# Performance work log

Hardware: AMD Instinct MI355X
Metric: run time of the kernel (lower is better)

Reference implementation:

```python
import jax, jax.numpy as jnp
import numpy as np

T, H, E, I, SI, TOP_K = 4096, 2048, 16, 1024, 4096, 1


def setup_inputs() -> dict:
    key = jax.random.key(0)
    ks = jax.random.split(key, 8)
    s_h = 1.0 / np.sqrt(H)
    s_i = 1.0 / np.sqrt(I)
    s_si = 1.0 / np.sqrt(SI)
    return {
        "hidden_states": jax.random.normal(ks[0], (T, H), jnp.float32),
        "router_w": jax.random.normal(ks[1], (E, H), jnp.float32) * s_h,
        "w_gate": jax.random.normal(ks[2], (E, H, I), jnp.float32) * s_h,
        "w_up": jax.random.normal(ks[3], (E, H, I), jnp.float32) * s_h,
        "w_down": jax.random.normal(ks[4], (E, I, H), jnp.float32) * s_i,
        "ws_gate": jax.random.normal(ks[5], (H, SI), jnp.float32) * s_h,
        "ws_up": jax.random.normal(ks[6], (H, SI), jnp.float32) * s_h,
        "ws_down": jax.random.normal(ks[7], (SI, H), jnp.float32) * s_si,
    }


def reference(hidden_states, router_w, w_gate, w_up, w_down, ws_gate, ws_up, ws_down):
    x = hidden_states  # [T, H]
    # Router: logits -> top-k -> sigmoid weights (Llama4RenormalizeMoeRoutingMethod)
    logits = jnp.einsum("th,eh->te", x, router_w)              # [T, E]
    top_vals, top_idx = jax.lax.top_k(logits, TOP_K)            # [T, K]
    weights = jax.nn.sigmoid(top_vals)                          # [T, K]
    # dispatch[t, e] = router weight if expert e selected for token t, else 0
    onehot = jax.nn.one_hot(top_idx, E, dtype=x.dtype)          # [T, K, E]
    dispatch = jnp.einsum("tke,tk->te", onehot, weights)        # [T, E]
    # Routed experts: router weight applied on input (commutes through the
    # linear gate/up projections as a per-(t,e) scalar applied before SiLU).
    g = jnp.einsum("th,ehi->tei", x, w_gate) * dispatch[:, :, None]  # [T, E, I]
    u = jnp.einsum("th,ehi->tei", x, w_up) * dispatch[:, :, None]    # [T, E, I]
    act = jax.nn.silu(g) * u                                          # [T, E, I]
    # Unselected experts contribute exactly 0 (act==0 there), so summing over
    # E in the down projection is the combine step.
    routed = jnp.einsum("tei,eih->th", act, w_down)             # [T, H]
    # Shared expert (SiLU-gated MLP on the unscaled hidden states)
    shared = (jax.nn.silu(x @ ws_gate) * (x @ ws_up)) @ ws_down  # [T, H]
    return shared + routed
```

## Files before the change

### kernel.cpp

```cpp
#include <hip/hip_runtime.h>
#include <hip/hip_bf16.h>

typedef unsigned short u16;
typedef unsigned int   u32;
typedef __attribute__((ext_vector_type(8))) short short8;
typedef __attribute__((ext_vector_type(4))) float f32x4;

#define T_TOK 4096
#define HDIM  2048
#define NEXP  16
#define IDIM  1024
#define SIDIM 4096
#define RCAP  6144
#define NTIL  48

#define O_WT      0u
#define O_EIDX    16384u
#define O_CNT     32768u
#define O_POS     32832u
#define O_PADOFF  32896u
#define O_TILEEXP 33024u
#define O_TOKROW  33280u
#define O_XBF     65536u
#define O_XSC     (O_XBF + 2u*T_TOK*HDIM)
#define O_ACTS    (O_XSC + 2u*RCAP*HDIM)
#define O_ACTR    (O_ACTS + 2u*T_TOK*SIDIM)

__device__ __forceinline__ u16 f2b(float f) {
  u32 u = __float_as_uint(f);
  u = (u + 0x7FFFu + ((u >> 16) & 1u)) >> 16;
  return (u16)u;
}

__global__ __launch_bounds__(256) void router_k(
    const float* __restrict__ x, const float* __restrict__ rw,
    float* __restrict__ wt, int* __restrict__ eidx, int* __restrict__ cnt) {
  int w = threadIdx.x >> 6, l = threadIdx.x & 63;
  int t = blockIdx.x * 4 + w;
  double acc[NEXP];
#pragma unroll
  for (int e = 0; e < NEXP; ++e) acc[e] = 0.0;
  const float* xp = x + (size_t)t * HDIM;
  for (int hb = 0; hb < HDIM; hb += 256) {
    float4 xv = *(const float4*)(xp + hb + l * 4);
#pragma unroll
    for (int e = 0; e < NEXP; ++e) {
      float4 wv = *(const float4*)(rw + (size_t)e * HDIM + hb + l * 4);
      acc[e] += (double)xv.x * wv.x + (double)xv.y * wv.y
              + (double)xv.z * wv.z + (double)xv.w * wv.w;
    }
  }
#pragma unroll
  for (int e = 0; e < NEXP; ++e) {
    double v = acc[e];
#pragma unroll
    for (int off = 32; off; off >>= 1) v += __shfl_xor(v, off, 64);
    acc[e] = v;
  }
  if (l == 0) {
    double best = acc[0]; int be = 0;
#pragma unroll
    for (int e = 1; e < NEXP; ++e) if (acc[e] > best) { best = acc[e]; be = e; }
    wt[t] = 1.0f / (1.0f + __expf(-(float)best));
    eidx[t] = be;
    atomicAdd(&cnt[be], 1);
  }
}

__global__ void scan_k(const int* __restrict__ cnt, int* __restrict__ pad_off,
                       int* __restrict__ tile_exp, int* __restrict__ pos,
                       int* __restrict__ tok_row) {
  if (threadIdx.x == 0) {
    for (int i = 0; i < 64; ++i) tile_exp[i] = -1;
    int run = 0;
    for (int e = 0; e < NEXP; ++e) {
      pad_off[e] = run;
      int pc = ((cnt[e] + 127) >> 7) << 7;
      for (int tt = run >> 7; tt < (run + pc) >> 7; ++tt) tile_exp[tt] = e;
      run += pc;
      pos[e] = 0;
    }
    pad_off[NEXP] = run;
  }
  for (int i = threadIdx.x; i < RCAP; i += 256) tok_row[i] = -1;
}

__global__ void assign_k(const int* __restrict__ eidx, const int* __restrict__ pad_off,
                         int* __restrict__ pos, int* __restrict__ tok_row) {
  int t = blockIdx.x * 256 + threadIdx.x;
  if (t >= T_TOK) return;
  int e = eidx[t];
  int r = atomicAdd(&pos[e], 1);
  tok_row[pad_off[e] + r] = t;
}

__global__ __launch_bounds__(256) void cvt_k(
    const float* __restrict__ x, const float* __restrict__ wt,
    const int* __restrict__ tok_row, u16* __restrict__ xbf, u16* __restrict__ xsc) {
  int row = blockIdx.x;
  int tid = threadIdx.x;
  if (row < T_TOK) {
    const float* src = x + (size_t)row * HDIM;
    u16* dst = xbf + (size_t)row * HDIM;
#pragma unroll
    for (int i = 0; i < 2; ++i) {
      int c = i * 1024 + tid * 4;
      float4 v = *(const float4*)(src + c);
      uint2 o;
      o.x = (u32)f2b(v.x) | ((u32)f2b(v.y) << 16);
      o.y = (u32)f2b(v.z) | ((u32)f2b(v.w) << 16);
      *(uint2*)(dst + c) = o;
    }
  } else {
    int g = row - T_TOK;
    u16* dst = xsc + (size_t)g * HDIM;
    int t = tok_row[g];
    if (t < 0) {
      uint2 z; z.x = 0u; z.y = 0u;
#pragma unroll
      for (int i = 0; i < 2; ++i) *(uint2*)(dst + i * 1024 + tid * 4) = z;
    } else {
      float s = wt[t];
      const float* src = x + (size_t)t * HDIM;
#pragma unroll
      for (int i = 0; i < 2; ++i) {
        int c = i * 1024 + tid * 4;
        float4 v = *(const float4*)(src + c);
        uint2 o;
        o.x = (u32)f2b(v.x * s) | ((u32)f2b(v.y * s) << 16);
        o.y = (u32)f2b(v.z * s) | ((u32)f2b(v.w * s) << 16);
        *(uint2*)(dst + c) = o;
      }
    }
  }
}


template<bool ROUTED>
__global__ __launch_bounds__(256) void gemm_gu(
    const u16* __restrict__ A, int lda,
    const float* __restrict__ Bg0, const float* __restrict__ Bu0, int ldb,
    int K, u16* __restrict__ act, int ldact,
    const int* __restrict__ tile_exp) {
  __shared__ __align__(16) u16 As[128 * 64];
  __shared__ __align__(16) u16 Bgs[64 * 72];
  __shared__ __align__(16) u16 Bus[64 * 72];
  const int tid = threadIdx.x;
  const int w = tid >> 6, l = tid & 63;
  const int wm = w >> 1, wn = w & 1;
  const int m0 = blockIdx.y * 128, n0 = blockIdx.x * 64;
  const float* Bg = Bg0;
  const float* Bu = Bu0;
  if (ROUTED) {
    int e = tile_exp[blockIdx.y];
    if (e < 0) return;
    size_t off = (size_t)e * (size_t)K * (size_t)ldb;
    Bg += off; Bu += off;
  }
  f32x4 accg[4][2], accu[4][2];
#pragma unroll
  for (int i = 0; i < 4; ++i)
#pragma unroll
    for (int j = 0; j < 2; ++j)
#pragma unroll
      for (int r = 0; r < 4; ++r) { accg[i][j][r] = 0.0f; accu[i][j][r] = 0.0f; }

  const int ra = tid >> 3;
  const int ca = (tid & 7) * 8;
  const u16* Ab = A + (size_t)m0 * lda;

  for (int k0 = 0; k0 < K; k0 += 64) {
    __syncthreads();
#pragma unroll
    for (int i = 0; i < 4; ++i) {
      int r = ra + 32 * i;
      int4 v = *(const int4*)(Ab + (size_t)r * lda + k0 + ca);
      *(int4*)&As[r * 64 + (ca ^ ((r & 7) * 8))] = v;
    }
    {
      const float* bp = Bg + (size_t)(k0 + w * 16) * ldb + n0 + l;
      u16 h[16];
#pragma unroll
      for (int i = 0; i < 16; ++i) h[i] = f2b(bp[(size_t)i * ldb]);
#pragma unroll
      for (int j = 0; j < 4; ++j) {
        uint2 v; v.x = (u32)h[4*j] | ((u32)h[4*j+1] << 16);
        v.y = (u32)h[4*j+2] | ((u32)h[4*j+3] << 16);
        *(uint2*)&Bgs[l * 72 + w * 16 + j * 4] = v;
      }
      bp = Bu + (size_t)(k0 + w * 16) * ldb + n0 + l;
#pragma unroll
      for (int i = 0; i < 16; ++i) h[i] = f2b(bp[(size_t)i * ldb]);
#pragma unroll
      for (int j = 0; j < 4; ++j) {
        uint2 v; v.x = (u32)h[4*j] | ((u32)h[4*j+1] << 16);
        v.y = (u32)h[4*j+2] | ((u32)h[4*j+3] << 16);
        *(uint2*)&Bus[l * 72 + w * 16 + j * 4] = v;
      }
    }
    __syncthreads();
#pragma unroll
    for (int kh = 0; kh < 2; ++kh) {
      short8 af[4];
#pragma unroll
      for (int mf = 0; mf < 4; ++mf) {
        int r = wm * 64 + mf * 16 + (l & 15);
        int c = (kh * 32 + (l >> 4) * 8) ^ ((r & 7) * 8);
        af[mf] = *(const short8*)&As[r * 64 + c];
      }
      short8 bgf[2], buf2[2];
#pragma unroll
      for (int nf = 0; nf < 2; ++nf) {
        int n = wn * 32 + nf * 16 + (l & 15);
        int c = kh * 32 + (l >> 4) * 8;
        bgf[nf]  = *(const short8*)&Bgs[n * 72 + c];
        buf2[nf] = *(const short8*)&Bus[n * 72 + c];
      }
#pragma unroll
      for (int mf = 0; mf < 4; ++mf)
#pragma unroll
        for (int nf = 0; nf < 2; ++nf) {
          accg[mf][nf] = __builtin_amdgcn_mfma_f32_16x16x32_bf16(af[mf], bgf[nf],  accg[mf][nf], 0, 0, 0);
          accu[mf][nf] = __builtin_amdgcn_mfma_f32_16x16x32_bf16(af[mf], buf2[nf], accu[mf][nf], 0, 0, 0);
        }
    }
  }
#pragma unroll
  for (int mf = 0; mf < 4; ++mf)
#pragma unroll
    for (int nf = 0; nf < 2; ++nf) {
      int col = n0 + wn * 32 + nf * 16 + (l & 15);
#pragma unroll
      for (int r = 0; r < 4; ++r) {
        int row = m0 + wm * 64 + mf * 16 + (l >> 4) * 4 + r;
        float g = accg[mf][nf][r], u = accu[mf][nf][r];
        float s = g / (1.0f + __expf(-g));
        act[(size_t)row * ldact + col] = f2b(s * u);
      }
    }
}

template<bool ROUTED>
__global__ __launch_bounds__(256) void gemm_down(
    const u16* __restrict__ A, int lda,
    const float* __restrict__ B0, int ldb, int K,
    float* __restrict__ out, int ldout,
    const int* __restrict__ tile_exp, const int* __restrict__ tok_row) {
  __shared__ __align__(16) u16 As[128 * 64];
  __shared__ __align__(16) u16 Bs[64 * 72];
  const int tid = threadIdx.x;
  const int w = tid >> 6, l = tid & 63;
  const int wm = w >> 1, wn = w & 1;
  const int m0 = blockIdx.y * 128, n0 = blockIdx.x * 64;
  const float* B = B0;
  if (ROUTED) {
    int e = tile_exp[blockIdx.y];
    if (e < 0) return;
    B += (size_t)e * (size_t)K * (size_t)ldb;
  }
  f32x4 acc[4][2];
#pragma unroll
  for (int i = 0; i < 4; ++i)
#pragma unroll
    for (int j = 0; j < 2; ++j)
#pragma unroll
      for (int r = 0; r < 4; ++r) acc[i][j][r] = 0.0f;

  const int ra = tid >> 3;
  const int ca = (tid & 7) * 8;
  const u16* Ab = A + (size_t)m0 * lda;

  for (int k0 = 0; k0 < K; k0 += 64) {
    __syncthreads();
#pragma unroll
    for (int i = 0; i < 4; ++i) {
      int r = ra + 32 * i;
      int4 v = *(const int4*)(Ab + (size_t)r * lda + k0 + ca);
      *(int4*)&As[r * 64 + (ca ^ ((r & 7) * 8))] = v;
    }
    {
      const float* bp = B + (size_t)(k0 + w * 16) * ldb + n0 + l;
      u16 h[16];
#pragma unroll
      for (int i = 0; i < 16; ++i) h[i] = f2b(bp[(size_t)i * ldb]);
#pragma unroll
      for (int j = 0; j < 4; ++j) {
        uint2 v; v.x = (u32)h[4*j] | ((u32)h[4*j+1] << 16);
        v.y = (u32)h[4*j+2] | ((u32)h[4*j+3] << 16);
        *(uint2*)&Bs[l * 72 + w * 16 + j * 4] = v;
      }
    }
    __syncthreads();
#pragma unroll
    for (int kh = 0; kh < 2; ++kh) {
      short8 af[4];
#pragma unroll
      for (int mf = 0; mf < 4; ++mf) {
        int r = wm * 64 + mf * 16 + (l & 15);
        int c = (kh * 32 + (l >> 4) * 8) ^ ((r & 7) * 8);
        af[mf] = *(const short8*)&As[r * 64 + c];
      }
      short8 bf[2];
#pragma unroll
      for (int nf = 0; nf < 2; ++nf) {
        int n = wn * 32 + nf * 16 + (l & 15);
        int c = kh * 32 + (l >> 4) * 8;
        bf[nf] = *(const short8*)&Bs[n * 72 + c];
      }
#pragma unroll
      for (int mf = 0; mf < 4; ++mf)
#pragma unroll
        for (int nf = 0; nf < 2; ++nf)
          acc[mf][nf] = __builtin_amdgcn_mfma_f32_16x16x32_bf16(af[mf], bf[nf], acc[mf][nf], 0, 0, 0);
    }
  }
#pragma unroll
  for (int mf = 0; mf < 4; ++mf)
#pragma unroll
    for (int nf = 0; nf < 2; ++nf) {
      int col = n0 + wn * 32 + nf * 16 + (l & 15);
#pragma unroll
      for (int r = 0; r < 4; ++r) {
        int grow = m0 + wm * 64 + mf * 16 + (l >> 4) * 4 + r;
        float v = acc[mf][nf][r];
        if (ROUTED) {
          int t = tok_row[grow];
          if (t >= 0) out[(size_t)t * ldout + col] += v;
        } else {
          out[(size_t)grow * ldout + col] = v;
        }
      }
    }
}

extern "C" void kernel_launch(void* const* d_in, const int* in_sizes, int n_in,
                              void* d_out, int out_size, void* d_ws, size_t ws_size,
                              hipStream_t stream) {
  const float* x   = (const float*)d_in[0];
  const float* rw  = (const float*)d_in[1];
  const float* wg  = (const float*)d_in[2];
  const float* wu  = (const float*)d_in[3];
  const float* wd  = (const float*)d_in[4];
  const float* wsg = (const float*)d_in[5];
  const float* wsu = (const float*)d_in[6];
  const float* wsd = (const float*)d_in[7];
  float* out = (float*)d_out;
  char* ws = (char*)d_ws;

  float* wt     = (float*)(ws + O_WT);
  int* eidx     = (int*)(ws + O_EIDX);
  int* cnt      = (int*)(ws + O_CNT);
  int* pos      = (int*)(ws + O_POS);
  int* pad_off  = (int*)(ws + O_PADOFF);
  int* tile_exp = (int*)(ws + O_TILEEXP);
  int* tok_row  = (int*)(ws + O_TOKROW);
  u16* xbf      = (u16*)(ws + O_XBF);
  u16* xsc      = (u16*)(ws + O_XSC);
  u16* acts     = (u16*)(ws + O_ACTS);
  u16* actr     = (u16*)(ws + O_ACTR);

  hipMemsetAsync(ws + O_CNT, 0, 128, stream);
  router_k<<<T_TOK / 4, 256, 0, stream>>>(x, rw, wt, eidx, cnt);
  scan_k<<<1, 256, 0, stream>>>(cnt, pad_off, tile_exp, pos, tok_row);
  assign_k<<<T_TOK / 256, 256, 0, stream>>>(eidx, pad_off, pos, tok_row);
  cvt_k<<<T_TOK + RCAP, 256, 0, stream>>>(x, wt, tok_row, xbf, xsc);
  gemm_gu<false><<<dim3(SIDIM / 64, T_TOK / 128), 256, 0, stream>>>(
      xbf, HDIM, wsg, wsu, SIDIM, HDIM, acts, SIDIM, nullptr);
  gemm_gu<true><<<dim3(IDIM / 64, NTIL), 256, 0, stream>>>(
      xsc, HDIM, wg, wu, IDIM, HDIM, actr, IDIM, tile_exp);
  gemm_down<false><<<dim3(HDIM / 64, T_TOK / 128), 256, 0, stream>>>(
      acts, SIDIM, wsd, HDIM, SIDIM, out, HDIM, nullptr, nullptr);
  gemm_down<true><<<dim3(HDIM / 64, NTIL), 256, 0, stream>>>(
      actr, IDIM, wd, HDIM, IDIM, out, HDIM, tile_exp, tok_row);
}
```

Before: 630.5 us.

## Pre-transpose weights to bf16 and stage tiles via global_load_lds

Adds a transpose-and-convert pass that writes each fp32 weight matrix as a K-contiguous bf16 copy in the workspace. The GEMMs then load A and B tiles straight into swizzled LDS with 16-byte global_load_lds, replacing per-element strided fp32 loads plus in-kernel conversion. The down-projection N tile grows from 64 to 128. The conversion still runs on every call and needs a much larger workspace, and falls back to the old path when the workspace is too small.

```diff
diff --git a/kernel.cpp b/kernel.cpp
--- a/kernel.cpp
+++ b/kernel.cpp
@@ -22,15 +22,27 @@
 #define O_TILEEXP 33024u
 #define O_TOKROW  33280u
 #define O_XBF     65536u
-#define O_XSC     (O_XBF + 2u*T_TOK*HDIM)
-#define O_ACTS    (O_XSC + 2u*RCAP*HDIM)
+#define O_XSC     (O_XBF  + 2u*T_TOK*HDIM)
+#define O_ACTS    (O_XSC  + 2u*RCAP*HDIM)
 #define O_ACTR    (O_ACTS + 2u*T_TOK*SIDIM)
+#define O_WSGT    (O_ACTR + 2u*RCAP*IDIM)
+#define O_WSUT    (O_WSGT + 2u*SIDIM*HDIM)
+#define O_WSDT    (O_WSUT + 2u*SIDIM*HDIM)
+#define O_WGT     (O_WSDT + 2u*HDIM*SIDIM)
+#define O_WUT     (O_WGT  + 2u*NEXP*IDIM*HDIM)
+#define O_WDT     (O_WUT  + 2u*NEXP*IDIM*HDIM)
+#define WS_SHARED_END (size_t)(O_WSDT + 2u*HDIM*SIDIM)
+#define WS_FULL_END   (size_t)(O_WDT  + 2u*NEXP*HDIM*IDIM)
 
 __device__ __forceinline__ u16 f2b(float f) {
   u32 u = __float_as_uint(f);
   u = (u + 0x7FFFu + ((u >> 16) & 1u)) >> 16;
   return (u16)u;
 }
+
+#define GLDS16(g, l) __builtin_amdgcn_global_load_lds( \
+    (const __attribute__((address_space(1))) void*)(g), \
+    (__attribute__((address_space(3))) void*)(l), 16, 0, 0)
 
 __global__ __launch_bounds__(256) void router_k(
     const float* __restrict__ x, const float* __restrict__ rw,
@@ -135,27 +147,51 @@
   }
 }
 
-
-template<bool ROUTED>
+__global__ __launch_bounds__(256) void tconv_k(
+    const float* __restrict__ src, u16* __restrict__ dst, int K, int N) {
+  size_t boff = (size_t)blockIdx.z * (size_t)K * N;
+  const float* sp = src + boff + (size_t)blockIdx.y * 32 * N + blockIdx.x * 256 + threadIdx.x;
+  u32 h[16];
+#pragma unroll
+  for (int i = 0; i < 16; ++i) {
+    float a = sp[(size_t)(2 * i) * N];
+    float b = sp[(size_t)(2 * i + 1) * N];
+    h[i] = (u32)f2b(a) | ((u32)f2b(b) << 16);
+  }
+  u16* dp = dst + boff + (size_t)(blockIdx.x * 256 + threadIdx.x) * K + blockIdx.y * 32;
+  uint4* dq = (uint4*)dp;
+  dq[0] = make_uint4(h[0], h[1], h[2], h[3]);
+  dq[1] = make_uint4(h[4], h[5], h[6], h[7]);
+  dq[2] = make_uint4(h[8], h[9], h[10], h[11]);
+  dq[3] = make_uint4(h[12], h[13], h[14], h[15]);
+}
+
+
+template<bool ROUTED, bool PRE>
 __global__ __launch_bounds__(256) void gemm_gu(
     const u16* __restrict__ A, int lda,
-    const float* __restrict__ Bg0, const float* __restrict__ Bu0, int ldb,
-    int K, u16* __restrict__ act, int ldact,
-    const int* __restrict__ tile_exp) {
+    const void* __restrict__ Bg0, const void* __restrict__ Bu0,
+    int ldb, size_t bstr, int K,
+    u16* __restrict__ act, int ldact, const int* __restrict__ tile_exp) {
   __shared__ __align__(16) u16 As[128 * 64];
-  __shared__ __align__(16) u16 Bgs[64 * 72];
-  __shared__ __align__(16) u16 Bus[64 * 72];
+  __shared__ __align__(16) u16 Bgs[PRE ? 64 * 64 : 64 * 72];
+  __shared__ __align__(16) u16 Bus[PRE ? 64 * 64 : 64 * 72];
   const int tid = threadIdx.x;
   const int w = tid >> 6, l = tid & 63;
   const int wm = w >> 1, wn = w & 1;
   const int m0 = blockIdx.y * 128, n0 = blockIdx.x * 64;
-  const float* Bg = Bg0;
-  const float* Bu = Bu0;
-  if (ROUTED) {
-    int e = tile_exp[blockIdx.y];
-    if (e < 0) return;
-    size_t off = (size_t)e * (size_t)K * (size_t)ldb;
-    Bg += off; Bu += off;
+  int e = 0;
+  if (ROUTED) { e = tile_exp[blockIdx.y]; if (e < 0) return; }
+  const u16 *BgT = nullptr, *BuT = nullptr;
+  const float *Bgf = nullptr, *Buf = nullptr;
+  if constexpr (PRE) {
+    size_t eo = ROUTED ? (size_t)e * bstr : 0;
+    BgT = (const u16*)Bg0 + eo + (size_t)n0 * ldb;
+    BuT = (const u16*)Bu0 + eo + (size_t)n0 * ldb;
+  } else {
+    size_t eo = ROUTED ? (size_t)e * bstr : 0;
+    Bgf = (const float*)Bg0 + eo;
+    Buf = (const float*)Bu0 + eo;
   }
   f32x4 accg[4][2], accu[4][2];
 #pragma unroll
@@ -164,21 +200,25 @@
     for (int j = 0; j < 2; ++j)
 #pragma unroll
       for (int r = 0; r < 4; ++r) { accg[i][j][r] = 0.0f; accu[i][j][r] = 0.0f; }
-
-  const int ra = tid >> 3;
-  const int ca = (tid & 7) * 8;
   const u16* Ab = A + (size_t)m0 * lda;
 
   for (int k0 = 0; k0 < K; k0 += 64) {
     __syncthreads();
 #pragma unroll
-    for (int i = 0; i < 4; ++i) {
-      int r = ra + 32 * i;
-      int4 v = *(const int4*)(Ab + (size_t)r * lda + k0 + ca);
-      *(int4*)&As[r * 64 + (ca ^ ((r & 7) * 8))] = v;
-    }
-    {
-      const float* bp = Bg + (size_t)(k0 + w * 16) * ldb + n0 + l;
+    for (int j = 0; j < 4; ++j) {
+      int c = j * 256 + tid, r = c >> 3, cc = c & 7;
+      GLDS16(Ab + (size_t)r * lda + k0 + ((cc ^ (r & 7)) * 8), &As[c * 8]);
+    }
+    if constexpr (PRE) {
+#pragma unroll
+      for (int j = 0; j < 2; ++j) {
+        int c = j * 256 + tid, r = c >> 3, cc = c & 7;
+        int sc = (cc ^ (r & 7)) * 8;
+        GLDS16(BgT + (size_t)r * ldb + k0 + sc, &Bgs[c * 8]);
+        GLDS16(BuT + (size_t)r * ldb + k0 + sc, &Bus[c * 8]);
+      }
+    } else {
+      const float* bp = Bgf + (size_t)(k0 + w * 16) * ldb + n0 + l;
       u16 h[16];
 #pragma unroll
       for (int i = 0; i < 16; ++i) h[i] = f2b(bp[(size_t)i * ldb]);
@@ -188,7 +228,7 @@
         v.y = (u32)h[4*j+2] | ((u32)h[4*j+3] << 16);
         *(uint2*)&Bgs[l * 72 + w * 16 + j * 4] = v;
       }
-      bp = Bu + (size_t)(k0 + w * 16) * ldb + n0 + l;
+      bp = Buf + (size_t)(k0 + w * 16) * ldb + n0 + l;
 #pragma unroll
       for (int i = 0; i < 16; ++i) h[i] = f2b(bp[(size_t)i * ldb]);
 #pragma unroll
@@ -201,20 +241,24 @@
     __syncthreads();
 #pragma unroll
     for (int kh = 0; kh < 2; ++kh) {
+      const int q = kh * 4 + (l >> 4);
       short8 af[4];
 #pragma unroll
       for (int mf = 0; mf < 4; ++mf) {
         int r = wm * 64 + mf * 16 + (l & 15);
-        int c = (kh * 32 + (l >> 4) * 8) ^ ((r & 7) * 8);
-        af[mf] = *(const short8*)&As[r * 64 + c];
+        af[mf] = *(const short8*)&As[r * 64 + ((q ^ (r & 7)) * 8)];
       }
       short8 bgf[2], buf2[2];
 #pragma unroll
       for (int nf = 0; nf < 2; ++nf) {
         int n = wn * 32 + nf * 16 + (l & 15);
-        int c = kh * 32 + (l >> 4) * 8;
-        bgf[nf]  = *(const short8*)&Bgs[n * 72 + c];
-        buf2[nf] = *(const short8*)&Bus[n * 72 + c];
+        if constexpr (PRE) {
+          bgf[nf]  = *(const short8*)&Bgs[n * 64 + ((q ^ (n & 7)) * 8)];
+          buf2[nf] = *(const short8*)&Bus[n * 64 + ((q ^ (n & 7)) * 8)];
+        } else {
+          bgf[nf]  = *(const short8*)&Bgs[n * 72 + q * 8];
+          buf2[nf] = *(const short8*)&Bus[n * 72 + q * 8];
+        }
       }
 #pragma unroll
       for (int mf = 0; mf < 4; ++mf)
@@ -240,46 +284,52 @@
     }
 }
 
-template<bool ROUTED>
+template<bool ROUTED, bool PRE>
 __global__ __launch_bounds__(256) void gemm_down(
     const u16* __restrict__ A, int lda,
-    const float* __restrict__ B0, int ldb, int K,
+    const void* __restrict__ B0, int ldb, size_t bstr, int K,
     float* __restrict__ out, int ldout,
     const int* __restrict__ tile_exp, const int* __restrict__ tok_row) {
+  constexpr int BN  = PRE ? 128 : 64;
+  constexpr int NFR = PRE ? 4 : 2;
   __shared__ __align__(16) u16 As[128 * 64];
-  __shared__ __align__(16) u16 Bs[64 * 72];
+  __shared__ __align__(16) u16 Bs[PRE ? 128 * 64 : 64 * 72];
   const int tid = threadIdx.x;
   const int w = tid >> 6, l = tid & 63;
   const int wm = w >> 1, wn = w & 1;
-  const int m0 = blockIdx.y * 128, n0 = blockIdx.x * 64;
-  const float* B = B0;
-  if (ROUTED) {
-    int e = tile_exp[blockIdx.y];
-    if (e < 0) return;
-    B += (size_t)e * (size_t)K * (size_t)ldb;
-  }
-  f32x4 acc[4][2];
+  const int m0 = blockIdx.y * 128, n0 = blockIdx.x * BN;
+  int e = 0;
+  if (ROUTED) { e = tile_exp[blockIdx.y]; if (e < 0) return; }
+  const u16* BT = nullptr; const float* Bf = nullptr;
+  if constexpr (PRE) {
+    BT = (const u16*)B0 + (ROUTED ? (size_t)e * bstr : 0) + (size_t)n0 * ldb;
+  } else {
+    Bf = (const float*)B0 + (ROUTED ? (size_t)e * bstr : 0);
+  }
+  f32x4 acc[4][NFR];
 #pragma unroll
   for (int i = 0; i < 4; ++i)
 #pragma unroll
-    for (int j = 0; j < 2; ++j)
+    for (int j = 0; j < NFR; ++j)
 #pragma unroll
       for (int r = 0; r < 4; ++r) acc[i][j][r] = 0.0f;
-
-  const int ra = tid >> 3;
-  const int ca = (tid & 7) * 8;
   const u16* Ab = A + (size_t)m0 * lda;
 
   for (int k0 = 0; k0 < K; k0 += 64) {
     __syncthreads();
 #pragma unroll
-    for (int i = 0; i < 4; ++i) {
-      int r = ra + 32 * i;
-      int4 v = *(const int4*)(Ab + (size_t)r * lda + k0 + ca);
-      *(int4*)&As[r * 64 + (ca ^ ((r & 7) * 8))] = v;
-    }
-    {
-      const float* bp = B + (size_t)(k0 + w * 16) * ldb + n0 + l;
+    for (int j = 0; j < 4; ++j) {
+      int c = j * 256 + tid, r = c >> 3, cc = c & 7;
+      GLDS16(Ab + (size_t)r * lda + k0 + ((cc ^ (r & 7)) * 8), &As[c * 8]);
+    }
+    if constexpr (PRE) {
+#pragma unroll
+      for (int j = 0; j < 4; ++j) {
+        int c = j * 256 + tid, r = c >> 3, cc = c & 7;
+        GLDS16(BT + (size_t)r * ldb + k0 + ((cc ^ (r & 7)) * 8), &Bs[c * 8]);
+      }
+    } else {
+      const float* bp = Bf + (size_t)(k0 + w * 16) * ldb + n0 + l;
       u16 h[16];
 #pragma unroll
       for (int i = 0; i < 16; ++i) h[i] = f2b(bp[(size_t)i * ldb]);
@@ -293,32 +343,32 @@
     __syncthreads();
 #pragma unroll
     for (int kh = 0; kh < 2; ++kh) {
+      const int q = kh * 4 + (l >> 4);
       short8 af[4];
 #pragma unroll
       for (int mf = 0; mf < 4; ++mf) {
         int r = wm * 64 + mf * 16 + (l & 15);
-        int c = (kh * 32 + (l >> 4) * 8) ^ ((r & 7) * 8);
-        af[mf] = *(const short8*)&As[r * 64 + c];
-      }
-      short8 bf[2];
-#pragma unroll
-      for (int nf = 0; nf < 2; ++nf) {
-        int n = wn * 32 + nf * 16 + (l & 15);
-        int c = kh * 32 + (l >> 4) * 8;
-        bf[nf] = *(const short8*)&Bs[n * 72 + c];
+        af[mf] = *(const short8*)&As[r * 64 + ((q ^ (r & 7)) * 8)];
+      }
+      short8 bf[NFR];
+#pragma unroll
+      for (int nf = 0; nf < NFR; ++nf) {
+        int n = wn * (BN / 2) + nf * 16 + (l & 15);
+        if constexpr (PRE) bf[nf] = *(const short8*)&Bs[n * 64 + ((q ^ (n & 7)) * 8)];
+        else               bf[nf] = *(const short8*)&Bs[n * 72 + q * 8];
       }
 #pragma unroll
       for (int mf = 0; mf < 4; ++mf)
 #pragma unroll
-        for (int nf = 0; nf < 2; ++nf)
+        for (int nf = 0; nf < NFR; ++nf)
           acc[mf][nf] = __builtin_amdgcn_mfma_f32_16x16x32_bf16(af[mf], bf[nf], acc[mf][nf], 0, 0, 0);
     }
   }
 #pragma unroll
   for (int mf = 0; mf < 4; ++mf)
 #pragma unroll
-    for (int nf = 0; nf < 2; ++nf) {
-      int col = n0 + wn * 32 + nf * 16 + (l & 15);
+    for (int nf = 0; nf < NFR; ++nf) {
+      int col = n0 + wn * (BN / 2) + nf * 16 + (l & 15);
 #pragma unroll
       for (int r = 0; r < 4; ++r) {
         int grow = m0 + wm * 64 + mf * 16 + (l >> 4) * 4 + r;
@@ -358,18 +408,57 @@
   u16* xsc      = (u16*)(ws + O_XSC);
   u16* acts     = (u16*)(ws + O_ACTS);
   u16* actr     = (u16*)(ws + O_ACTR);
+  u16* wsgT     = (u16*)(ws + O_WSGT);
+  u16* wsuT     = (u16*)(ws + O_WSUT);
+  u16* wsdT     = (u16*)(ws + O_WSDT);
+  u16* wgT      = (u16*)(ws + O_WGT);
+  u16* wuT      = (u16*)(ws + O_WUT);
+  u16* wdT      = (u16*)(ws + O_WDT);
+
+  const bool preS = ws_size >= WS_SHARED_END;
+  const bool preR = ws_size >= WS_FULL_END;
 
   hipMemsetAsync(ws + O_CNT, 0, 128, stream);
+  if (preS) {
+    tconv_k<<<dim3(SIDIM / 256, HDIM / 32, 1), 256, 0, stream>>>(wsg, wsgT, HDIM, SIDIM);
+    tconv_k<<<dim3(SIDIM / 256, HDIM / 32, 1), 256, 0, stream>>>(wsu, wsuT, HDIM, SIDIM);
+    tconv_k<<<dim3(HDIM / 256, SIDIM / 32, 1), 256, 0, stream>>>(wsd, wsdT, SIDIM, HDIM);
+  }
+  if (preR) {
+    tconv_k<<<dim3(IDIM / 256, HDIM / 32, NEXP), 256, 0, stream>>>(wg, wgT, HDIM, IDIM);
+    tconv_k<<<dim3(IDIM / 256, HDIM / 32, NEXP), 256, 0, stream>>>(wu, wuT, HDIM, IDIM);
+    tconv_k<<<dim3(HDIM / 256, IDIM / 32, NEXP), 256, 0, stream>>>(wd, wdT, IDIM, HDIM);
+  }
   router_k<<<T_TOK / 4, 256, 0, stream>>>(x, rw, wt, eidx, cnt);
   scan_k<<<1, 256, 0, stream>>>(cnt, pad_off, tile_exp, pos, tok_row);
   assign_k<<<T_TOK / 256, 256, 0, stream>>>(eidx, pad_off, pos, tok_row);
   cvt_k<<<T_TOK + RCAP, 256, 0, stream>>>(x, wt, tok_row, xbf, xsc);
-  gemm_gu<false><<<dim3(SIDIM / 64, T_TOK / 128), 256, 0, stream>>>(
-      xbf, HDIM, wsg, wsu, SIDIM, HDIM, acts, SIDIM, nullptr);
-  gemm_gu<true><<<dim3(IDIM / 64, NTIL), 256, 0, stream>>>(
-      xsc, HDIM, wg, wu, IDIM, HDIM, actr, IDIM, tile_exp);
-  gemm_down<false><<<dim3(HDIM / 64, T_TOK / 128), 256, 0, stream>>>(
-      acts, SIDIM, wsd, HDIM, SIDIM, out, HDIM, nullptr, nullptr);
-  gemm_down<true><<<dim3(HDIM / 64, NTIL), 256, 0, stream>>>(
-      actr, IDIM, wd, HDIM, IDIM, out, HDIM, tile_exp, tok_row);
-}
+
+  if (preS)
+    gemm_gu<false, true><<<dim3(SIDIM / 64, T_TOK / 128), 256, 0, stream>>>(
+        xbf, HDIM, wsgT, wsuT, HDIM, 0, HDIM, acts, SIDIM, nullptr);
+  else
+    gemm_gu<false, false><<<dim3(SIDIM / 64, T_TOK / 128), 256, 0, stream>>>(
+        xbf, HDIM, wsg, wsu, SIDIM, 0, HDIM, acts, SIDIM, nullptr);
+
+  if (preR)
+    gemm_gu<true, true><<<dim3(IDIM / 64, NTIL), 256, 0, stream>>>(
+        xsc, HDIM, wgT, wuT, HDIM, (size_t)IDIM * HDIM, HDIM, actr, IDIM, tile_exp);
+  else
+    gemm_gu<true, false><<<dim3(IDIM / 64, NTIL), 256, 0, stream>>>(
+        xsc, HDIM, wg, wu, IDIM, (size_t)HDIM * IDIM, HDIM, actr, IDIM, tile_exp);
+
+  if (preS)
+    gemm_down<false, true><<<dim3(HDIM / 128, T_TOK / 128), 256, 0, stream>>>(
+        acts, SIDIM, wsdT, SIDIM, 0, SIDIM, out, HDIM, nullptr, nullptr);
+  else
+    gemm_down<false, false><<<dim3(HDIM / 64, T_TOK / 128), 256, 0, stream>>>(
+        acts, SIDIM, wsd, HDIM, 0, SIDIM, out, HDIM, nullptr, nullptr);
+
+  if (preR)
+    gemm_down<true, true><<<dim3(HDIM / 128, NTIL), 256, 0, stream>>>(
+        actr, IDIM, wdT, IDIM, (size_t)HDIM * IDIM, IDIM, out, HDIM, tile_exp, tok_row);
+  else
+    gemm_down<true, false><<<dim3(HDIM / 64, NTIL), 256, 0, stream>>>(
+        actr, IDIM, wd, HDIM, (size_t)IDIM * HDIM, IDIM, out, HDIM, tile_exp, tok_row);
+}
```

New measurement: 673.2 us. 1.07x slower.
